# Optimization experiments

Measured on AMD Instinct MI355X. Metric: run time of the kernel, lower is better.

The kernel has to match this reference:

```python
import jax, jax.numpy as jnp
import numpy as np

TEMPERATURE = 0.1
EPS_NORM = 1e-12  # torch F.normalize eps
EPS_LOSS = 1e-8


def setup_inputs() -> dict:
    key = jax.random.key(0)
    k1, k2 = jax.random.split(key)
    N, D, K = 8192, 512, 64
    features = jax.random.normal(k1, (N, D), dtype=jnp.float32)
    cluster_assignments = jax.random.randint(k2, (N,), 0, K, dtype=jnp.int64)
    return {"features": features, "cluster_assignments": cluster_assignments}


def reference(features, cluster_assignments):
    # L2 normalize rows (torch.nn.functional.normalize, p=2, dim=1)
    norm = jnp.linalg.norm(features, axis=1, keepdims=True)
    features_norm = features / jnp.maximum(norm, EPS_NORM)
    # pairwise cosine similarity scaled by temperature -> [N, N]
    sim = jnp.einsum('id,jd->ij', features_norm, features_norm) / TEMPERATURE
    exp_sim = jnp.exp(sim)
    mask = (cluster_assignments[None, :] == cluster_assignments[:, None]).astype(exp_sim.dtype)
    pos_sum = jnp.sum(exp_sim * mask, axis=1, keepdims=True)
    neg_sum = jnp.sum(exp_sim * (1.0 - mask), axis=1, keepdims=True)
    loss = -jnp.log(pos_sum / (pos_sum + neg_sum + EPS_LOSS))
    return jnp.sum(loss)  # reduction='sum'
```

## Files before the change

kernel.cpp:

```cpp
#include <hip/hip_runtime.h>
#include <hip/hip_bf16.h>
#include <stdint.h>

#define N 8192
#define D 512
#define TILE 128
#define BK 64
#define NKC (D / BK)
#define NTB (N / TILE)
#define NBLK (NTB * (NTB + 1) / 2)
#define PANEL_BYTES (TILE * D)
#define KCHUNK_BYTES (TILE * BK)

typedef long long i64;
typedef __attribute__((ext_vector_type(4))) float f32x4;

__device__ __forceinline__ void gload_lds16(const void* gp, const void* lp) {
    auto g = (const __attribute__((address_space(1))) void*)(uintptr_t)gp;
    auto l = (__attribute__((address_space(3))) void*)(uintptr_t)lp;
    __builtin_amdgcn_global_load_lds(g, l, 16, 0, 0);
}


__global__ void cc_normalize(const float* __restrict__ F, uint8_t* __restrict__ Fn2,
                             float* __restrict__ out) {
    if (blockIdx.x == 0 && threadIdx.x == 0) out[0] = 0.0f;
    const int row  = blockIdx.x * 4 + (threadIdx.x >> 6);
    const int lane = threadIdx.x & 63;
    const float* p = F + (size_t)row * D + lane * 8;
    float4 a = *(const float4*)p;
    float4 b = *(const float4*)(p + 4);
    float ss = a.x*a.x + a.y*a.y + a.z*a.z + a.w*a.w
             + b.x*b.x + b.y*b.y + b.z*b.z + b.w*b.w;
    #pragma unroll
    for (int m = 32; m; m >>= 1) ss += __shfl_xor(ss, m, 64);
    const float inv = 16.0f / fmaxf(sqrtf(ss), 1e-12f);
    int lo = 0, hi = 0;
    lo = __builtin_amdgcn_cvt_pk_fp8_f32(a.x*inv, a.y*inv, lo, false);
    lo = __builtin_amdgcn_cvt_pk_fp8_f32(a.z*inv, a.w*inv, lo, true);
    hi = __builtin_amdgcn_cvt_pk_fp8_f32(b.x*inv, b.y*inv, hi, false);
    hi = __builtin_amdgcn_cvt_pk_fp8_f32(b.z*inv, b.w*inv, hi, true);
    const size_t idx = (size_t)(row >> 7) * PANEL_BYTES + (size_t)lane * 1024 + (row & 127) * 8;
    *(int2*)(Fn2 + idx) = make_int2(lo, hi);
}

__global__ __launch_bounds__(256, 4)
void cc_gemm(const uint8_t* __restrict__ Fn2, const int* __restrict__ cl,
             float* __restrict__ Pt, float* __restrict__ Pp) {
    __shared__ __align__(16) uint8_t As[2][KCHUNK_BYTES];
    __shared__ __align__(16) uint8_t Bs[2][KCHUNK_BYTES];
    __shared__ int crow[TILE], ccol[TILE];
    __shared__ float rsum[2][TILE][2];
    __shared__ float csum[2][TILE][2];

    const int tid  = threadIdx.x;
    const int wave = tid >> 6;
    const int lane = tid & 63;

    int rem = blockIdx.x, bm = 0;
    while (rem >= NTB - bm) { rem -= NTB - bm; ++bm; }
    const int bn = bm + rem;
    const bool diag = (bm == bn);

    if (tid < TILE)            crow[tid]        = cl[bm * TILE + tid];
    else                       ccol[tid - TILE] = cl[bn * TILE + (tid - TILE)];

    const int wr = wave >> 1, wc = wave & 1;
    const int q   = lane >> 4;
    const int n15 = lane & 15;

    f32x4 acc[4][4];
    #pragma unroll
    for (int t = 0; t < 4; ++t)
        #pragma unroll
        for (int u = 0; u < 4; ++u) acc[t][u] = (f32x4)(0.0f);

    const uint8_t* Ag = Fn2 + (size_t)bm * PANEL_BYTES;
    const uint8_t* Bg = Fn2 + (size_t)bn * PANEL_BYTES;

    #pragma unroll
    for (int i = 0; i < 2; ++i) {
        const int off = (wave * 2 + i) * 1024;
        gload_lds16(Ag + off + lane * 16, &As[0][off]);
        gload_lds16(Bg + off + lane * 16, &Bs[0][off]);
    }

    for (int kc = 0; kc < NKC; ++kc) {
        const int b = kc & 1;
        __syncthreads();
        if (kc + 1 < NKC) {
            const uint8_t* ga = Ag + (kc + 1) * KCHUNK_BYTES;
            const uint8_t* gb = Bg + (kc + 1) * KCHUNK_BYTES;
            #pragma unroll
            for (int i = 0; i < 2; ++i) {
                const int off = (wave * 2 + i) * 1024;
                gload_lds16(ga + off + lane * 16, &As[b ^ 1][off]);
                gload_lds16(gb + off + lane * 16, &Bs[b ^ 1][off]);
            }
        }
        #pragma unroll
        for (int ks = 0; ks < 2; ++ks) {
            const int base = ks * 4096 + q * 1024 + n15 * 8;
            i64 af[4], bfr[4];
            #pragma unroll
            for (int t = 0; t < 4; ++t)
                af[t] = *(const i64*)&As[b][base + (wr * 64 + t * 16) * 8];
            #pragma unroll
            for (int u = 0; u < 4; ++u)
                bfr[u] = *(const i64*)&Bs[b][base + (wc * 64 + u * 16) * 8];
            #pragma unroll
            for (int t = 0; t < 4; ++t)
                #pragma unroll
                for (int u = 0; u < 4; ++u)
                    acc[t][u] = __builtin_amdgcn_mfma_f32_16x16x32_fp8_fp8(af[t], bfr[u], acc[t][u], 0, 0, 0);
        }
    }

    const float SC = 0.05635527503472514f;
    int cc[4];
    #pragma unroll
    for (int u = 0; u < 4; ++u) cc[u] = ccol[wc * 64 + u * 16 + n15];

    float ce[4] = {0.f, 0.f, 0.f, 0.f};
    float cp[4] = {0.f, 0.f, 0.f, 0.f};

    #pragma unroll
    for (int t = 0; t < 4; ++t) {
        #pragma unroll
        for (int r = 0; r < 4; ++r) {
            const int lr  = wr * 64 + t * 16 + q * 4 + r;
            const int myc = crow[lr];
            float te = 0.0f, tp = 0.0f;
            #pragma unroll
            for (int u = 0; u < 4; ++u) {
                const float e  = exp2f(acc[t][u][r] * SC);
                const float ep = (cc[u] == myc) ? e : 0.0f;
                te += e;  tp += ep;
                ce[u] += e;  cp[u] += ep;
            }
            #pragma unroll
            for (int m = 1; m < 16; m <<= 1) {
                te += __shfl_xor(te, m, 64);
                tp += __shfl_xor(tp, m, 64);
            }
            if (n15 == 0) { rsum[wc][lr][0] = te; rsum[wc][lr][1] = tp; }
        }
    }

    if (!diag) {
        #pragma unroll
        for (int u = 0; u < 4; ++u) {
            float e = ce[u], p = cp[u];
            e += __shfl_xor(e, 16, 64);  p += __shfl_xor(p, 16, 64);
            e += __shfl_xor(e, 32, 64);  p += __shfl_xor(p, 32, 64);
            if (lane < 16) {
                const int lc = wc * 64 + u * 16 + n15;
                csum[wr][lc][0] = e;  csum[wr][lc][1] = p;
            }
        }
    }

    __syncthreads();
    if (tid < TILE) {
        const float te = rsum[0][tid][0] + rsum[1][tid][0];
        const float tp = rsum[0][tid][1] + rsum[1][tid][1];
        const size_t o = (size_t)bn * N + bm * TILE + tid;
        Pt[o] = te;  Pp[o] = tp;
    } else if (!diag) {
        const int c = tid - TILE;
        const float te = csum[0][c][0] + csum[1][c][0];
        const float tp = csum[0][c][1] + csum[1][c][1];
        const size_t o = (size_t)bm * N + bn * TILE + c;
        Pt[o] = te;  Pp[o] = tp;
    }
}

__global__ void cc_finalize(const float* __restrict__ Pt, const float* __restrict__ Pp,
                            float* __restrict__ out) {
    __shared__ float red[4];
    const int i = blockIdx.x * 256 + threadIdx.x;
    float tv = 0.0f, pv = 0.0f;
    #pragma unroll 8
    for (int s = 0; s < NTB; ++s) {
        tv += Pt[(size_t)s * N + i];
        pv += Pp[(size_t)s * N + i];
    }
    float l = __logf(tv + 1e-8f) - __logf(pv);
    #pragma unroll
    for (int m = 32; m; m >>= 1) l += __shfl_xor(l, m, 64);
    const int wv = threadIdx.x >> 6, lane = threadIdx.x & 63;
    if (lane == 0) red[wv] = l;
    __syncthreads();
    if (threadIdx.x == 0) atomicAdd(out, red[0] + red[1] + red[2] + red[3]);
}

extern "C" void kernel_launch(void* const* d_in, const int* in_sizes, int n_in,
                              void* d_out, int out_size, void* d_ws, size_t ws_size,
                              hipStream_t stream) {
    const float* F  = (const float*)d_in[0];
    const int*   cl = (const int*)d_in[1];
    float* out = (float*)d_out;

    uint8_t* Fn2 = (uint8_t*)d_ws;
    float* Pt  = (float*)((char*)d_ws + (size_t)N * D);
    float* Pp  = Pt + (size_t)NTB * N;

    cc_normalize<<<N / 4, 256, 0, stream>>>(F, Fn2, out);
    cc_gemm<<<NBLK, 256, 0, stream>>>(Fn2, cl, Pt, Pp);
    cc_finalize<<<N / 256, 256, 0, stream>>>(Pt, Pp, out);
}
```

Baseline: 128.3 us.

## Triple-buffer GEMM k-chunks with explicit vmcnt waits and reuse LDS for sums

Switches the fp8 GEMM main loop from double to triple buffering, prefetching two chunks ahead. Each step waits with a partial s_waitcnt vmcnt plus a raw barrier, so the newest chunk's loads can stay in flight. Reduction scratch now aliases the staging buffers to save LDS, and occupancy bounds drop from 4 to 3 blocks. This trades occupancy and hand-written waitcnt correctness risk for deeper latency hiding.

```diff
diff --git a/kernel.cpp b/kernel.cpp
--- a/kernel.cpp
+++ b/kernel.cpp
@@ -20,7 +20,6 @@
     auto l = (__attribute__((address_space(3))) void*)(uintptr_t)lp;
     __builtin_amdgcn_global_load_lds(g, l, 16, 0, 0);
 }
-
 
 __global__ void cc_normalize(const float* __restrict__ F, uint8_t* __restrict__ Fn2,
                              float* __restrict__ out) {
@@ -44,14 +43,15 @@
     *(int2*)(Fn2 + idx) = make_int2(lo, hi);
 }
 
-__global__ __launch_bounds__(256, 4)
+__global__ __launch_bounds__(256, 3)
 void cc_gemm(const uint8_t* __restrict__ Fn2, const int* __restrict__ cl,
              float* __restrict__ Pt, float* __restrict__ Pp) {
-    __shared__ __align__(16) uint8_t As[2][KCHUNK_BYTES];
-    __shared__ __align__(16) uint8_t Bs[2][KCHUNK_BYTES];
+    __shared__ __align__(16) uint8_t smem[6 * KCHUNK_BYTES];
     __shared__ int crow[TILE], ccol[TILE];
-    __shared__ float rsum[2][TILE][2];
-    __shared__ float csum[2][TILE][2];
+    uint8_t* As = smem;
+    uint8_t* Bs = smem + 3 * KCHUNK_BYTES;
+    float (*rsum)[TILE][2] = (float (*)[TILE][2])(smem);
+    float (*csum)[TILE][2] = (float (*)[TILE][2])(smem + 4096);
 
     const int tid  = threadIdx.x;
     const int wave = tid >> 6;
@@ -78,36 +78,38 @@
     const uint8_t* Ag = Fn2 + (size_t)bm * PANEL_BYTES;
     const uint8_t* Bg = Fn2 + (size_t)bn * PANEL_BYTES;
 
-    #pragma unroll
-    for (int i = 0; i < 2; ++i) {
-        const int off = (wave * 2 + i) * 1024;
-        gload_lds16(Ag + off + lane * 16, &As[0][off]);
-        gload_lds16(Bg + off + lane * 16, &Bs[0][off]);
-    }
-
+    auto stage = [&](int kc, int buf) {
+        const uint8_t* ga = Ag + kc * KCHUNK_BYTES;
+        const uint8_t* gb = Bg + kc * KCHUNK_BYTES;
+        #pragma unroll
+        for (int i = 0; i < 2; ++i) {
+            const int off = (wave * 2 + i) * 1024;
+            gload_lds16(ga + off + lane * 16, As + buf * KCHUNK_BYTES + off);
+            gload_lds16(gb + off + lane * 16, Bs + buf * KCHUNK_BYTES + off);
+        }
+    };
+
+    stage(0, 0);
+    stage(1, 1);
+
+    #pragma unroll
     for (int kc = 0; kc < NKC; ++kc) {
-        const int b = kc & 1;
-        __syncthreads();
-        if (kc + 1 < NKC) {
-            const uint8_t* ga = Ag + (kc + 1) * KCHUNK_BYTES;
-            const uint8_t* gb = Bg + (kc + 1) * KCHUNK_BYTES;
-            #pragma unroll
-            for (int i = 0; i < 2; ++i) {
-                const int off = (wave * 2 + i) * 1024;
-                gload_lds16(ga + off + lane * 16, &As[b ^ 1][off]);
-                gload_lds16(gb + off + lane * 16, &Bs[b ^ 1][off]);
-            }
-        }
+        const int b = kc % 3;
+        if (kc < NKC - 1)
+            asm volatile("s_waitcnt vmcnt(4) lgkmcnt(0)\n\ts_barrier" ::: "memory");
+        else
+            asm volatile("s_waitcnt vmcnt(0) lgkmcnt(0)\n\ts_barrier" ::: "memory");
+        if (kc + 2 < NKC) stage(kc + 2, (kc + 2) % 3);
         #pragma unroll
         for (int ks = 0; ks < 2; ++ks) {
-            const int base = ks * 4096 + q * 1024 + n15 * 8;
+            const int base = b * KCHUNK_BYTES + ks * 4096 + q * 1024 + n15 * 8;
             i64 af[4], bfr[4];
             #pragma unroll
             for (int t = 0; t < 4; ++t)
-                af[t] = *(const i64*)&As[b][base + (wr * 64 + t * 16) * 8];
+                af[t] = *(const i64*)&As[base + (wr * 64 + t * 16) * 8];
             #pragma unroll
             for (int u = 0; u < 4; ++u)
-                bfr[u] = *(const i64*)&Bs[b][base + (wc * 64 + u * 16) * 8];
+                bfr[u] = *(const i64*)&Bs[base + (wc * 64 + u * 16) * 8];
             #pragma unroll
             for (int t = 0; t < 4; ++t)
                 #pragma unroll
@@ -115,6 +117,8 @@
                     acc[t][u] = __builtin_amdgcn_mfma_f32_16x16x32_fp8_fp8(af[t], bfr[u], acc[t][u], 0, 0, 0);
         }
     }
+
+    __syncthreads();
 
     const float SC = 0.05635527503472514f;
     int cc[4];
@@ -150,12 +154,12 @@
     if (!diag) {
         #pragma unroll
         for (int u = 0; u < 4; ++u) {
-            float e = ce[u], p = cp[u];
-            e += __shfl_xor(e, 16, 64);  p += __shfl_xor(p, 16, 64);
-            e += __shfl_xor(e, 32, 64);  p += __shfl_xor(p, 32, 64);
+            float e = ce[u], p2 = cp[u];
+            e += __shfl_xor(e, 16, 64);  p2 += __shfl_xor(p2, 16, 64);
+            e += __shfl_xor(e, 32, 64);  p2 += __shfl_xor(p2, 32, 64);
             if (lane < 16) {
                 const int lc = wc * 64 + u * 16 + n15;
-                csum[wr][lc][0] = e;  csum[wr][lc][1] = p;
+                csum[wr][lc][0] = e;  csum[wr][lc][1] = p2;
             }
         }
     }
```

After: 125.0 us. 2.6% less time.
